# Kernel optimization log

Measured on AMD Instinct MI355X. Metric: run time of the kernel, lower is better.

The kernel has to match this reference:

```python
import jax, jax.numpy as jnp
import numpy as np

N = 20000           # graph nodes == vocab_size
E_RAND = 160000     # random edges (avg degree 8)
E = E_RAND + N      # + self loops (dgl.add_self_loop)
B, S, D = 16, 512, 768
IN_DIM, HID, HEADS = 4, 16, 8
GRID = 10010
NEG_SLOPE = 0.2


def _zero_row0(t):
    # padding_idx=0 in nn.Embedding -> row 0 is zeros
    return t.at[0].set(0.0)


def setup_inputs() -> dict:
    key = jax.random.key(0)
    ks = jax.random.split(key, 20)
    self_loops = jnp.arange(N, dtype=jnp.int64 if jax.config.x64_enabled else jnp.int32)
    edge_src = jax.random.randint(ks[0], (E,), 0, N).at[E_RAND:].set(self_loops)
    edge_dst = jax.random.randint(ks[1], (E,), 0, N).at[E_RAND:].set(self_loops)
    inp = {
        "trj_token": jax.random.randint(ks[2], (B, S), 0, N),
        "min_list": jax.random.randint(ks[3], (B, S), 0, 1441),
        "weekday_list": jax.random.randint(ks[4], (B, S), 0, 8),
        "day_list": jax.random.randint(ks[5], (B, S), 0, 367),
        "grid_list": jax.random.randint(ks[6], (B, S), 0, GRID),
        "poi_list": jax.random.randint(ks[7], (B, S), 0, 5),
        "edge_src": edge_src,
        "edge_dst": edge_dst,
        "feature": jax.random.normal(ks[8], (N, IN_DIM), jnp.float32),
        "W_src1": jax.random.normal(ks[9], (IN_DIM, HEADS, HID), jnp.float32) * 0.3,
        "W_dst1": jax.random.normal(ks[10], (IN_DIM, HEADS, HID), jnp.float32) * 0.3,
        "attn1": jax.random.normal(ks[11], (HEADS, HID), jnp.float32) * 0.3,
        "W_src2": jax.random.normal(ks[12], (HEADS * HID, 1, D), jnp.float32) * 0.05,
        "W_dst2": jax.random.normal(ks[13], (HEADS * HID, 1, D), jnp.float32) * 0.05,
        "attn2": jax.random.normal(ks[14], (1, D), jnp.float32) * 0.05,
        "grid_table": _zero_row0(jax.random.normal(ks[15], (GRID, D), jnp.float32)),
        "daytime_table": _zero_row0(jax.random.normal(ks[16], (1441, D), jnp.float32)),
        "weekday_table": _zero_row0(jax.random.normal(ks[17], (8, D), jnp.float32)),
        "day_table": _zero_row0(jax.random.normal(ks[18], (367, D), jnp.float32)),
    }
    return inp


def gatv2_layer(x, es, ed, W_s, W_d, attn):
    # GATv2: score_e = attn . leaky_relu(Wsrc x[src] + Wdst x[dst]); edge-softmax over dst
    hs = jnp.einsum('nd,dhf->nhf', x, W_s)           # [N,H,F]
    hd = jnp.einsum('nd,dhf->nhf', x, W_d)           # [N,H,F]
    e = jax.nn.leaky_relu(hs[es] + hd[ed], NEG_SLOPE)  # [E,H,F]
    score = jnp.einsum('ehf,hf->eh', e, attn)        # [E,H]
    m = jax.lax.stop_gradient(jax.ops.segment_max(score, ed, num_segments=N))
    ex = jnp.exp(score - m[ed])
    denom = jax.ops.segment_sum(ex, ed, num_segments=N)  # [N,H]
    alpha = ex / denom[ed]                           # [E,H]
    msg = alpha[..., None] * hs[es]                  # [E,H,F]
    return jax.ops.segment_sum(msg, ed, num_segments=N)  # [N,H,F]


def positional_embedding(seq_len, d_model):
    pos = jnp.arange(seq_len, dtype=jnp.float32)[:, None]
    div = jnp.exp(jnp.arange(0, d_model, 2, dtype=jnp.float32) * (-np.log(10000.0) / d_model))
    pe = jnp.zeros((seq_len, d_model), jnp.float32)
    pe = pe.at[:, 0::2].set(jnp.sin(pos * div))
    pe = pe.at[:, 1::2].set(jnp.cos(pos * div))
    return pe[None]  # [1,S,D]


def reference(trj_token, min_list, weekday_list, day_list, grid_list, poi_list,
              edge_src, edge_dst, feature,
              W_src1, W_dst1, attn1, W_src2, W_dst2, attn2,
              grid_table, daytime_table, weekday_table, day_table):
    # GAT2: two GATv2 layers over the road-network graph
    h1 = gatv2_layer(feature, edge_src, edge_dst, W_src1, W_dst1, attn1)   # [N,8,16]
    h1 = jax.nn.elu(h1.reshape(N, HEADS * HID))                            # concat heads
    h2 = gatv2_layer(h1, edge_src, edge_dst, W_src2, W_dst2, attn2)        # [N,1,768]
    node_emb = h2[:, 0, :]                                                 # [N,768]

    token = node_emb[trj_token]                                            # [B,S,D]
    time_emb = (weekday_table[weekday_list]
                + daytime_table[min_list]
                + day_table[day_list])
    grid_emb = grid_table[grid_list]
    pe = positional_embedding(trj_token.shape[1], D)
    return pe + token + time_emb + grid_emb
```

## Files before the change

### kernel.cpp

```cpp
#include <hip/hip_runtime.h>
#include <hip/hip_bf16.h>

#define N_NODES 20000
#define N_EDGES 180000
#define D_OUT   768
#define D_H1    128
#define B_SZ    16
#define S_LEN   512
#define NEG_SLOPE_C 0.2f

typedef __attribute__((ext_vector_type(8))) short bf16x8;
typedef __attribute__((ext_vector_type(4))) float f32x4;

__device__ __forceinline__ float leaky1(float x){ return x >= 0.0f ? x : NEG_SLOPE_C * x; }
__device__ __forceinline__ unsigned short f2bf(float x){
  union { __hip_bfloat16 h; unsigned short u; } v; v.h = __float2bfloat16(x); return v.u;
}
__device__ __forceinline__ float bf2f(unsigned short u){
  return __uint_as_float(((unsigned)u) << 16);
}
__device__ __forceinline__ float4 bf4_to_f4(ushort4 u){
  return make_float4(bf2f(u.x), bf2f(u.y), bf2f(u.z), bf2f(u.w));
}
__device__ __forceinline__ ushort4 f4_to_bf4(float4 v){
  ushort4 u; u.x=f2bf(v.x); u.y=f2bf(v.y); u.z=f2bf(v.z); u.w=f2bf(v.w); return u;
}

__device__ __forceinline__ float score12(const float4&u0,const float4&u1,const float4&u2,
                                         const float4&h0,const float4&h1,const float4&h2v,
                                         const float4&a0,const float4&a1,const float4&a2){
  return leaky1(u0.x+h0.x)*a0.x + leaky1(u0.y+h0.y)*a0.y
       + leaky1(u0.z+h0.z)*a0.z + leaky1(u0.w+h0.w)*a0.w
       + leaky1(u1.x+h1.x)*a1.x + leaky1(u1.y+h1.y)*a1.y
       + leaky1(u1.z+h1.z)*a1.z + leaky1(u1.w+h1.w)*a1.w
       + leaky1(u2.x+h2v.x)*a2.x + leaky1(u2.y+h2v.y)*a2.y
       + leaky1(u2.z+h2v.z)*a2.z + leaky1(u2.w+h2v.w)*a2.w;
}
__device__ __forceinline__ void rescale_if(float mn, float&m, float&den,
                                           float4&a0,float4&a1,float4&a2){
  if(mn > m){
    float r = expf(m - mn);
    den *= r;
    a0.x*=r; a0.y*=r; a0.z*=r; a0.w*=r;
    a1.x*=r; a1.y*=r; a1.z*=r; a1.w*=r;
    a2.x*=r; a2.y*=r; a2.z*=r; a2.w*=r;
    m = mn;
  }
}
__device__ __forceinline__ void axpy12(float w, const float4&u0,const float4&u1,const float4&u2,
                                       float4&a0,float4&a1,float4&a2){
  a0.x+=w*u0.x; a0.y+=w*u0.y; a0.z+=w*u0.z; a0.w+=w*u0.w;
  a1.x+=w*u1.x; a1.y+=w*u1.y; a1.z+=w*u1.z; a1.w+=w*u1.w;
  a2.x+=w*u2.x; a2.y+=w*u2.y; a2.z+=w*u2.z; a2.w+=w*u2.w;
}
__device__ __forceinline__ void edge_pair(const unsigned short* __restrict__ hs2,
    const int* __restrict__ es, const int* __restrict__ eidx, int k, int l,
    const float4&h0,const float4&h1,const float4&h2v,
    const float4&w0,const float4&w1,const float4&w2,
    float&m,float&den,float4&a0,float4&a1,float4&a2){
  int e0=eidx[k], e1=eidx[k+1];
  const ushort4* p0=(const ushort4*)(hs2+(size_t)es[e0]*D_OUT);
  const ushort4* p1=(const ushort4*)(hs2+(size_t)es[e1]*D_OUT);
  float4 u0=bf4_to_f4(p0[l]),u1=bf4_to_f4(p0[64+l]),u2=bf4_to_f4(p0[128+l]);
  float4 v0=bf4_to_f4(p1[l]),v1=bf4_to_f4(p1[64+l]),v2=bf4_to_f4(p1[128+l]);
  float s0=score12(u0,u1,u2,h0,h1,h2v,w0,w1,w2);
  float s1=score12(v0,v1,v2,h0,h1,h2v,w0,w1,w2);
  #pragma unroll
  for(int off=1; off<64; off<<=1){ s0+=__shfl_xor(s0,off,64); s1+=__shfl_xor(s1,off,64); }
  float mn=fmaxf(m,fmaxf(s0,s1));
  rescale_if(mn,m,den,a0,a1,a2);
  float q0=expf(s0-m), q1=expf(s1-m);
  den+=q0+q1;
  axpy12(q0,u0,u1,u2,a0,a1,a2);
  axpy12(q1,v0,v1,v2,a0,a1,a2);
}
__device__ __forceinline__ void edge_one(const unsigned short* __restrict__ hs2,
    const int* __restrict__ es, const int* __restrict__ eidx, int k, int l,
    const float4&h0,const float4&h1,const float4&h2v,
    const float4&w0,const float4&w1,const float4&w2,
    float&m,float&den,float4&a0,float4&a1,float4&a2){
  int e0=eidx[k];
  const ushort4* p0=(const ushort4*)(hs2+(size_t)es[e0]*D_OUT);
  float4 u0=bf4_to_f4(p0[l]),u1=bf4_to_f4(p0[64+l]),u2=bf4_to_f4(p0[128+l]);
  float s0=score12(u0,u1,u2,h0,h1,h2v,w0,w1,w2);
  #pragma unroll
  for(int off=1; off<64; off<<=1) s0+=__shfl_xor(s0,off,64);
  float mn=fmaxf(m,s0);
  rescale_if(mn,m,den,a0,a1,a2);
  float q0=expf(s0-m);
  den+=q0;
  axpy12(q0,u0,u1,u2,a0,a1,a2);
}

__global__ void k_count(const int* __restrict__ ed, int* __restrict__ deg){
  int e = blockIdx.x*256 + threadIdx.x;
  if(e < N_EDGES) atomicAdd(&deg[ed[e]], 1);
}

__global__ void k_scan(const int* __restrict__ deg, int* __restrict__ row_ptr, int* __restrict__ cursor){
  __shared__ int part[256];
  int t = threadIdx.x;
  const int CH = (N_NODES + 255) / 256;
  int base = t * CH;
  int s = 0;
  for(int i=0;i<CH;i++){ int n = base+i; if(n < N_NODES) s += deg[n]; }
  part[t] = s;
  __syncthreads();
  for(int off=1; off<256; off<<=1){
    int v = (t >= off) ? part[t-off] : 0;
    __syncthreads();
    part[t] += v;
    __syncthreads();
  }
  int run = (t==0) ? 0 : part[t-1];
  for(int i=0;i<CH;i++){
    int n = base+i;
    if(n < N_NODES){ row_ptr[n] = run; cursor[n] = run; run += deg[n]; }
  }
  if(t == 255) row_ptr[N_NODES] = run;
}

__global__ void k_scatter(const int* __restrict__ ed, int* __restrict__ cursor, int* __restrict__ eidx){
  int e = blockIdx.x*256 + threadIdx.x;
  if(e < N_EDGES){
    int pos = atomicAdd(&cursor[ed[e]], 1);
    eidx[pos] = e;
  }
}

__global__ void k_gemm1(const float* __restrict__ feat, const float* __restrict__ Ws,
                        const float* __restrict__ Wd,
                        unsigned short* __restrict__ hs1, unsigned short* __restrict__ hd1){
  int idx = blockIdx.x*256 + threadIdx.x;
  if(idx >= N_NODES*D_H1) return;
  int n = idx >> 7, hf = idx & 127;
  float f0 = feat[n*4+0], f1 = feat[n*4+1], f2 = feat[n*4+2], f3 = feat[n*4+3];
  hs1[idx] = f2bf(f0*Ws[hf] + f1*Ws[128+hf] + f2*Ws[256+hf] + f3*Ws[384+hf]);
  hd1[idx] = f2bf(f0*Wd[hf] + f1*Wd[128+hf] + f2*Wd[256+hf] + f3*Wd[384+hf]);
}

__global__ void k_fused1(const unsigned short* __restrict__ hs1, const unsigned short* __restrict__ hd1,
                         const int* __restrict__ es, const int* __restrict__ row_ptr,
                         const int* __restrict__ eidx, const float* __restrict__ attn1,
                         unsigned short* __restrict__ h1){
  int node = blockIdx.x*4 + (threadIdx.x >> 6);
  int l = threadIdx.x & 63;
  if(node >= N_NODES) return;
  int rp = row_ptr[node], re = row_ptr[node+1];
  float hda = bf2f(hd1[(size_t)node*D_H1 + l]);
  float hdb = bf2f(hd1[(size_t)node*D_H1 + 64 + l]);
  float awa = attn1[l], awb = attn1[64 + l];
  float m0 = -INFINITY, m1 = -INFINITY;
  float d0 = 0.f, d1 = 0.f, a0 = 0.f, a1 = 0.f;
  int k = rp;
  for(; k+1 < re; k += 2){
    int e0 = eidx[k], e1 = eidx[k+1];
    int s0 = es[e0],  s1 = es[e1];
    float xa0 = bf2f(hs1[(size_t)s0*D_H1 + l]);
    float xb0 = bf2f(hs1[(size_t)s0*D_H1 + 64 + l]);
    float xa1 = bf2f(hs1[(size_t)s1*D_H1 + l]);
    float xb1 = bf2f(hs1[(size_t)s1*D_H1 + 64 + l]);
    float ta0 = leaky1(xa0 + hda) * awa;
    float tb0 = leaky1(xb0 + hdb) * awb;
    float ta1 = leaky1(xa1 + hda) * awa;
    float tb1 = leaky1(xb1 + hdb) * awb;
    #pragma unroll
    for(int off=1; off<16; off<<=1){
      ta0 += __shfl_xor(ta0, off, 64);
      tb0 += __shfl_xor(tb0, off, 64);
      ta1 += __shfl_xor(ta1, off, 64);
      tb1 += __shfl_xor(tb1, off, 64);
    }
    float mn0 = fmaxf(m0, fmaxf(ta0, ta1));
    float mn1 = fmaxf(m1, fmaxf(tb0, tb1));
    float r0 = expf(m0 - mn0), r1 = expf(m1 - mn1);
    float wa0 = expf(ta0 - mn0), wa1 = expf(ta1 - mn0);
    float wb0 = expf(tb0 - mn1), wb1 = expf(tb1 - mn1);
    d0 = d0*r0 + wa0 + wa1;
    d1 = d1*r1 + wb0 + wb1;
    a0 = a0*r0 + wa0*xa0 + wa1*xa1;
    a1 = a1*r1 + wb0*xb0 + wb1*xb1;
    m0 = mn0; m1 = mn1;
  }
  if(k < re){
    int e = eidx[k]; int s = es[e];
    float xa = bf2f(hs1[(size_t)s*D_H1 + l]);
    float xb = bf2f(hs1[(size_t)s*D_H1 + 64 + l]);
    float t0 = leaky1(xa + hda) * awa;
    float t1 = leaky1(xb + hdb) * awb;
    #pragma unroll
    for(int off=1; off<16; off<<=1){
      t0 += __shfl_xor(t0, off, 64);
      t1 += __shfl_xor(t1, off, 64);
    }
    float mn0 = fmaxf(m0, t0), mn1 = fmaxf(m1, t1);
    float r0 = expf(m0 - mn0), r1 = expf(m1 - mn1);
    float w0 = expf(t0 - mn0), w1 = expf(t1 - mn1);
    d0 = d0*r0 + w0;      d1 = d1*r1 + w1;
    a0 = a0*r0 + w0*xa;   a1 = a1*r1 + w1*xb;
    m0 = mn0; m1 = mn1;
  }
  float v0 = a0 / d0, v1 = a1 / d1;
  v0 = v0 > 0.f ? v0 : expm1f(v0);
  v1 = v1 > 0.f ? v1 : expm1f(v1);
  h1[(size_t)node*D_H1 + l]      = f2bf(v0);
  h1[(size_t)node*D_H1 + 64 + l] = f2bf(v1);
}

__global__ void k_wprep(const float* __restrict__ Ws, const float* __restrict__ Wd,
                        unsigned short* __restrict__ WtS, unsigned short* __restrict__ WtD){
  int i = blockIdx.x*256 + threadIdx.x;
  if(i >= D_OUT*D_H1) return;
  int c = i >> 7, k = i & 127;
  WtS[i] = f2bf(Ws[(size_t)k*D_OUT + c]);
  WtD[i] = f2bf(Wd[(size_t)k*D_OUT + c]);
}

__global__ __launch_bounds__(256) void k_gemm2m(const unsigned short* __restrict__ h1b,
                        const unsigned short* __restrict__ WtS, const unsigned short* __restrict__ WtD,
                        unsigned short* __restrict__ hs2, unsigned short* __restrict__ hd2){
  int wave = threadIdx.x >> 6, lane = threadIdx.x & 63;
  int wr = wave >> 1, wc = wave & 1;
  int m0 = blockIdx.x*64 + wr*32;
  int c0 = blockIdx.y*128 + wc*64;
  int lr = lane & 15, lk = lane >> 4;

  f32x4 acc[2][4][2];
  #pragma unroll
  for(int a=0;a<2;a++)
    #pragma unroll
    for(int j=0;j<4;j++)
      #pragma unroll
      for(int mmat=0;mmat<2;mmat++)
        acc[a][j][mmat] = (f32x4){0.f,0.f,0.f,0.f};

  int ra0 = m0 + lr;      if(ra0 > N_NODES-1) ra0 = N_NODES-1;
  int ra1 = m0 + 16 + lr; if(ra1 > N_NODES-1) ra1 = N_NODES-1;
  const unsigned short* pa0 = h1b + (size_t)ra0*D_H1 + lk*8;
  const unsigned short* pa1 = h1b + (size_t)ra1*D_H1 + lk*8;

  #pragma unroll
  for(int t=0;t<4;t++){
    bf16x8 a0 = *(const bf16x8*)(pa0 + t*32);
    bf16x8 a1 = *(const bf16x8*)(pa1 + t*32);
    #pragma unroll
    for(int j=0;j<4;j++){
      size_t bo = (size_t)(c0 + j*16 + lr)*D_H1 + t*32 + lk*8;
      bf16x8 bs = *(const bf16x8*)(WtS + bo);
      bf16x8 bd = *(const bf16x8*)(WtD + bo);
      acc[0][j][0] = __builtin_amdgcn_mfma_f32_16x16x32_bf16(a0, bs, acc[0][j][0], 0, 0, 0);
      acc[1][j][0] = __builtin_amdgcn_mfma_f32_16x16x32_bf16(a1, bs, acc[1][j][0], 0, 0, 0);
      acc[0][j][1] = __builtin_amdgcn_mfma_f32_16x16x32_bf16(a0, bd, acc[0][j][1], 0, 0, 0);
      acc[1][j][1] = __builtin_amdgcn_mfma_f32_16x16x32_bf16(a1, bd, acc[1][j][1], 0, 0, 0);
    }
  }

  #pragma unroll
  for(int a=0;a<2;a++){
    #pragma unroll
    for(int r=0;r<4;r++){
      int row = m0 + a*16 + lk*4 + r;
      if(row < N_NODES){
        size_t base = (size_t)row*D_OUT;
        #pragma unroll
        for(int j=0;j<4;j++){
          int col = c0 + j*16 + lr;
          hs2[base + col] = f2bf(acc[a][j][0][r]);
          hd2[base + col] = f2bf(acc[a][j][1][r]);
        }
      }
    }
  }
}

__global__ __launch_bounds__(256) void k_fused2(const unsigned short* __restrict__ hs2,
                         const unsigned short* __restrict__ hd2,
                         const int* __restrict__ es, const int* __restrict__ row_ptr,
                         const int* __restrict__ eidx, const float* __restrict__ attn2,
                         unsigned short* __restrict__ h2){
  int wv = threadIdx.x >> 6, l = threadIdx.x & 63;
  int nA = blockIdx.x*8 + wv*2;
  int nB = nA + 1;
  if(nA >= N_NODES) return;
  bool hasB = (nB < N_NODES);

  const float4* pa = (const float4*)attn2;
  float4 aw0 = pa[l], aw1 = pa[64+l], aw2 = pa[128+l];
  const ushort4* pdA = (const ushort4*)(hd2 + (size_t)nA*D_OUT);
  float4 hA0 = bf4_to_f4(pdA[l]), hA1 = bf4_to_f4(pdA[64+l]), hA2 = bf4_to_f4(pdA[128+l]);
  float4 hB0, hB1, hB2;
  if(hasB){
    const ushort4* pdB = (const ushort4*)(hd2 + (size_t)nB*D_OUT);
    hB0 = bf4_to_f4(pdB[l]); hB1 = bf4_to_f4(pdB[64+l]); hB2 = bf4_to_f4(pdB[128+l]);
  } else { hB0 = hB1 = hB2 = make_float4(0,0,0,0); }

  int kA = row_ptr[nA], reA = row_ptr[nA+1];
  int kB = hasB ? row_ptr[nB] : 0, reB = hasB ? row_ptr[nB+1] : 0;

  float mA = -INFINITY, dA = 0.f;
  float mB = -INFINITY, dB = 0.f;
  float4 aA0 = make_float4(0,0,0,0), aA1 = aA0, aA2 = aA0;
  float4 aB0 = aA0, aB1 = aA0, aB2 = aA0;

  while(kA+1 < reA && kB+1 < reB){
    int eA0 = eidx[kA], eA1 = eidx[kA+1], eB0 = eidx[kB], eB1 = eidx[kB+1];
    const ushort4* p0 = (const ushort4*)(hs2 + (size_t)es[eA0]*D_OUT);
    const ushort4* p1 = (const ushort4*)(hs2 + (size_t)es[eA1]*D_OUT);
    const ushort4* p2 = (const ushort4*)(hs2 + (size_t)es[eB0]*D_OUT);
    const ushort4* p3 = (const ushort4*)(hs2 + (size_t)es[eB1]*D_OUT);
    float4 uA0=bf4_to_f4(p0[l]), uA1=bf4_to_f4(p0[64+l]), uA2=bf4_to_f4(p0[128+l]);
    float4 vA0=bf4_to_f4(p1[l]), vA1=bf4_to_f4(p1[64+l]), vA2=bf4_to_f4(p1[128+l]);
    float4 uB0=bf4_to_f4(p2[l]), uB1=bf4_to_f4(p2[64+l]), uB2=bf4_to_f4(p2[128+l]);
    float4 vB0=bf4_to_f4(p3[l]), vB1=bf4_to_f4(p3[64+l]), vB2=bf4_to_f4(p3[128+l]);
    float s0 = score12(uA0,uA1,uA2, hA0,hA1,hA2, aw0,aw1,aw2);
    float s1 = score12(vA0,vA1,vA2, hA0,hA1,hA2, aw0,aw1,aw2);
    float s2 = score12(uB0,uB1,uB2, hB0,hB1,hB2, aw0,aw1,aw2);
    float s3 = score12(vB0,vB1,vB2, hB0,hB1,hB2, aw0,aw1,aw2);
    #pragma unroll
    for(int off=1; off<64; off<<=1){
      s0 += __shfl_xor(s0, off, 64);
      s1 += __shfl_xor(s1, off, 64);
      s2 += __shfl_xor(s2, off, 64);
      s3 += __shfl_xor(s3, off, 64);
    }
    float mnA = fmaxf(mA, fmaxf(s0, s1));
    rescale_if(mnA, mA, dA, aA0, aA1, aA2);
    float qa0 = expf(s0 - mA), qa1 = expf(s1 - mA);
    dA += qa0 + qa1;
    axpy12(qa0, uA0,uA1,uA2, aA0,aA1,aA2);
    axpy12(qa1, vA0,vA1,vA2, aA0,aA1,aA2);
    float mnB = fmaxf(mB, fmaxf(s2, s3));
    rescale_if(mnB, mB, dB, aB0, aB1, aB2);
    float qb0 = expf(s2 - mB), qb1 = expf(s3 - mB);
    dB += qb0 + qb1;
    axpy12(qb0, uB0,uB1,uB2, aB0,aB1,aB2);
    axpy12(qb1, vB0,vB1,vB2, aB0,aB1,aB2);
    kA += 2; kB += 2;
  }
  while(kA+1 < reA){ edge_pair(hs2, es, eidx, kA, l, hA0,hA1,hA2, aw0,aw1,aw2, mA,dA,aA0,aA1,aA2); kA += 2; }
  while(kB+1 < reB){ edge_pair(hs2, es, eidx, kB, l, hB0,hB1,hB2, aw0,aw1,aw2, mB,dB,aB0,aB1,aB2); kB += 2; }
  if(kA < reA) edge_one(hs2, es, eidx, kA, l, hA0,hA1,hA2, aw0,aw1,aw2, mA,dA,aA0,aA1,aA2);
  if(kB < reB) edge_one(hs2, es, eidx, kB, l, hB0,hB1,hB2, aw0,aw1,aw2, mB,dB,aB0,aB1,aB2);

  {
    float rd = 1.f/dA;
    ushort4* po = (ushort4*)(h2 + (size_t)nA*D_OUT);
    aA0.x*=rd; aA0.y*=rd; aA0.z*=rd; aA0.w*=rd;
    aA1.x*=rd; aA1.y*=rd; aA1.z*=rd; aA1.w*=rd;
    aA2.x*=rd; aA2.y*=rd; aA2.z*=rd; aA2.w*=rd;
    po[l] = f4_to_bf4(aA0); po[64+l] = f4_to_bf4(aA1); po[128+l] = f4_to_bf4(aA2);
  }
  if(hasB){
    float rd = 1.f/dB;
    ushort4* po = (ushort4*)(h2 + (size_t)nB*D_OUT);
    aB0.x*=rd; aB0.y*=rd; aB0.z*=rd; aB0.w*=rd;
    aB1.x*=rd; aB1.y*=rd; aB1.z*=rd; aB1.w*=rd;
    aB2.x*=rd; aB2.y*=rd; aB2.z*=rd; aB2.w*=rd;
    po[l] = f4_to_bf4(aB0); po[64+l] = f4_to_bf4(aB1); po[128+l] = f4_to_bf4(aB2);
  }
}

__global__ __launch_bounds__(192) void k_out(const unsigned short* __restrict__ h2,
    const int* __restrict__ tok, const int* __restrict__ mins, const int* __restrict__ wkd,
    const int* __restrict__ dayl, const int* __restrict__ grd,
    const float* __restrict__ grid_t, const float* __restrict__ dayt_t,
    const float* __restrict__ week_t, const float* __restrict__ day_t,
    float* __restrict__ out){
  int bs = blockIdx.x;
  int t  = threadIdx.x;
  int s  = bs & (S_LEN-1);
  int tk = tok[bs], mn = mins[bs], wk = wkd[bs], dy = dayl[bs], gr = grd[bs];
  float4 r = bf4_to_f4(((const ushort4*)(h2 + (size_t)tk*D_OUT))[t]);
  float4 v;
  v = ((const float4*)(week_t + (size_t)wk*D_OUT))[t]; r.x+=v.x; r.y+=v.y; r.z+=v.z; r.w+=v.w;
  v = ((const float4*)(dayt_t + (size_t)mn*D_OUT))[t]; r.x+=v.x; r.y+=v.y; r.z+=v.z; r.w+=v.w;
  v = ((const float4*)(day_t  + (size_t)dy*D_OUT))[t]; r.x+=v.x; r.y+=v.y; r.z+=v.z; r.w+=v.w;
  v = ((const float4*)(grid_t + (size_t)gr*D_OUT))[t]; r.x+=v.x; r.y+=v.y; r.z+=v.z; r.w+=v.w;
  const float K = 0.011992630692677313f;
  float d0 = expf(-K * (float)(4*t));
  float d1 = expf(-K * (float)(4*t+2));
  float sf = (float)s;
  r.x += sinf(sf*d0); r.y += cosf(sf*d0);
  r.z += sinf(sf*d1); r.w += cosf(sf*d1);
  ((float4*)(out + (size_t)bs*D_OUT))[t] = r;
}

extern "C" void kernel_launch(void* const* d_in, const int* in_sizes, int n_in,
                              void* d_out, int out_size, void* d_ws, size_t ws_size,
                              hipStream_t stream) {
  const int*   trj   = (const int*)  d_in[0];
  const int*   mins  = (const int*)  d_in[1];
  const int*   wkd   = (const int*)  d_in[2];
  const int*   dayl  = (const int*)  d_in[3];
  const int*   grd   = (const int*)  d_in[4];
  const int*   es    = (const int*)  d_in[6];
  const int*   ed    = (const int*)  d_in[7];
  const float* feat  = (const float*)d_in[8];
  const float* Ws1   = (const float*)d_in[9];
  const float* Wd1   = (const float*)d_in[10];
  const float* attn1 = (const float*)d_in[11];
  const float* Ws2   = (const float*)d_in[12];
  const float* Wd2   = (const float*)d_in[13];
  const float* attn2 = (const float*)d_in[14];
  const float* gridt = (const float*)d_in[15];
  const float* daytt = (const float*)d_in[16];
  const float* weekt = (const float*)d_in[17];
  const float* dayt  = (const float*)d_in[18];
  float* out = (float*)d_out;

  char* ws = (char*)d_ws;
  size_t off = 0;
  auto alloc = [&](size_t bytes)->char*{
    char* p = ws + off;
    off += bytes;
    off = (off + 255) & ~(size_t)255;
    return p;
  };
  unsigned short* hs1 = (unsigned short*)alloc((size_t)N_NODES*D_H1*2);
  unsigned short* hd1 = (unsigned short*)alloc((size_t)N_NODES*D_H1*2);
  unsigned short* h1  = (unsigned short*)alloc((size_t)N_NODES*D_H1*2);
  unsigned short* WtS = (unsigned short*)alloc((size_t)D_OUT*D_H1*2);
  unsigned short* WtD = (unsigned short*)alloc((size_t)D_OUT*D_H1*2);
  unsigned short* hs2 = (unsigned short*)alloc((size_t)N_NODES*D_OUT*2);
  unsigned short* hd2 = (unsigned short*)alloc((size_t)N_NODES*D_OUT*2);
  unsigned short* h2  = (unsigned short*)alloc((size_t)N_NODES*D_OUT*2);
  int* deg      = (int*)alloc((size_t)N_NODES*4);
  int* row_ptr  = (int*)alloc((size_t)(N_NODES+1)*4);
  int* cursor   = (int*)alloc((size_t)N_NODES*4);
  int* eidx     = (int*)alloc((size_t)N_EDGES*4);

  hipMemsetAsync(deg, 0, (size_t)N_NODES*4, stream);
  k_count  <<<(N_EDGES+255)/256, 256, 0, stream>>>(ed, deg);
  k_scan   <<<1, 256, 0, stream>>>(deg, row_ptr, cursor);
  k_scatter<<<(N_EDGES+255)/256, 256, 0, stream>>>(ed, cursor, eidx);

  k_gemm1 <<<(N_NODES*D_H1)/256, 256, 0, stream>>>(feat, Ws1, Wd1, hs1, hd1);
  k_fused1<<<(N_NODES+3)/4, 256, 0, stream>>>(hs1, hd1, es, row_ptr, eidx, attn1, h1);

  k_wprep <<<(D_OUT*D_H1+255)/256, 256, 0, stream>>>(Ws2, Wd2, WtS, WtD);
  dim3 g2((N_NODES+63)/64, D_OUT/128);
  k_gemm2m<<<g2, 256, 0, stream>>>(h1, WtS, WtD, hs2, hd2);
  k_fused2<<<(N_NODES+7)/8, 256, 0, stream>>>(hs2, hd2, es, row_ptr, eidx, attn2, h2);

  k_out<<<B_SZ*S_LEN, 192, 0, stream>>>(h2, trj, mins, wkd, dayl, grd,
                                        gridt, daytt, weekt, dayt, out);
}
```

Baseline: 363.6 us.

## Store source ids in CSR, preload neighbor lists per wave, one node per wave

The scatter step now writes the source node id directly into the CSR array, which removes the eidx→es double indirection in both aggregation kernels. Each wave loads up to 64 neighbor ids with one coalesced read and hands them out with shuffles, falling back to global loads when the degree exceeds 64. k_fused2 goes from two interleaved nodes per wave to one node per wave with twice as many blocks. This trades the memory-level parallelism of interleaving two nodes for simpler code and more waves.

```diff
diff --git a/kernel.cpp b/kernel.cpp
--- a/kernel.cpp
+++ b/kernel.cpp
@@ -53,14 +53,13 @@
   a1.x+=w*u1.x; a1.y+=w*u1.y; a1.z+=w*u1.z; a1.w+=w*u1.w;
   a2.x+=w*u2.x; a2.y+=w*u2.y; a2.z+=w*u2.z; a2.w+=w*u2.w;
 }
-__device__ __forceinline__ void edge_pair(const unsigned short* __restrict__ hs2,
-    const int* __restrict__ es, const int* __restrict__ eidx, int k, int l,
+__device__ __forceinline__ void f2_pair(const unsigned short* __restrict__ hs2,
+    int s0i, int s1i, int l,
     const float4&h0,const float4&h1,const float4&h2v,
     const float4&w0,const float4&w1,const float4&w2,
     float&m,float&den,float4&a0,float4&a1,float4&a2){
-  int e0=eidx[k], e1=eidx[k+1];
-  const ushort4* p0=(const ushort4*)(hs2+(size_t)es[e0]*D_OUT);
-  const ushort4* p1=(const ushort4*)(hs2+(size_t)es[e1]*D_OUT);
+  const ushort4* p0=(const ushort4*)(hs2+(size_t)s0i*D_OUT);
+  const ushort4* p1=(const ushort4*)(hs2+(size_t)s1i*D_OUT);
   float4 u0=bf4_to_f4(p0[l]),u1=bf4_to_f4(p0[64+l]),u2=bf4_to_f4(p0[128+l]);
   float4 v0=bf4_to_f4(p1[l]),v1=bf4_to_f4(p1[64+l]),v2=bf4_to_f4(p1[128+l]);
   float s0=score12(u0,u1,u2,h0,h1,h2v,w0,w1,w2);
@@ -74,13 +73,12 @@
   axpy12(q0,u0,u1,u2,a0,a1,a2);
   axpy12(q1,v0,v1,v2,a0,a1,a2);
 }
-__device__ __forceinline__ void edge_one(const unsigned short* __restrict__ hs2,
-    const int* __restrict__ es, const int* __restrict__ eidx, int k, int l,
+__device__ __forceinline__ void f2_one(const unsigned short* __restrict__ hs2,
+    int s0i, int l,
     const float4&h0,const float4&h1,const float4&h2v,
     const float4&w0,const float4&w1,const float4&w2,
     float&m,float&den,float4&a0,float4&a1,float4&a2){
-  int e0=eidx[k];
-  const ushort4* p0=(const ushort4*)(hs2+(size_t)es[e0]*D_OUT);
+  const ushort4* p0=(const ushort4*)(hs2+(size_t)s0i*D_OUT);
   float4 u0=bf4_to_f4(p0[l]),u1=bf4_to_f4(p0[64+l]),u2=bf4_to_f4(p0[128+l]);
   float s0=score12(u0,u1,u2,h0,h1,h2v,w0,w1,w2);
   #pragma unroll
@@ -120,11 +118,12 @@
   if(t == 255) row_ptr[N_NODES] = run;
 }
 
-__global__ void k_scatter(const int* __restrict__ ed, int* __restrict__ cursor, int* __restrict__ eidx){
+__global__ void k_scatter(const int* __restrict__ es, const int* __restrict__ ed,
+                          int* __restrict__ cursor, int* __restrict__ sidx){
   int e = blockIdx.x*256 + threadIdx.x;
   if(e < N_EDGES){
     int pos = atomicAdd(&cursor[ed[e]], 1);
-    eidx[pos] = e;
+    sidx[pos] = es[e];
   }
 }
 
@@ -140,22 +139,27 @@
 }
 
 __global__ void k_fused1(const unsigned short* __restrict__ hs1, const unsigned short* __restrict__ hd1,
-                         const int* __restrict__ es, const int* __restrict__ row_ptr,
-                         const int* __restrict__ eidx, const float* __restrict__ attn1,
+                         const int* __restrict__ row_ptr, const int* __restrict__ sidx,
+                         const float* __restrict__ attn1,
                          unsigned short* __restrict__ h1){
   int node = blockIdx.x*4 + (threadIdx.x >> 6);
   int l = threadIdx.x & 63;
   if(node >= N_NODES) return;
   int rp = row_ptr[node], re = row_ptr[node+1];
+  int deg = re - rp;
   float hda = bf2f(hd1[(size_t)node*D_H1 + l]);
   float hdb = bf2f(hd1[(size_t)node*D_H1 + 64 + l]);
   float awa = attn1[l], awb = attn1[64 + l];
   float m0 = -INFINITY, m1 = -INFINITY;
   float d0 = 0.f, d1 = 0.f, a0 = 0.f, a1 = 0.f;
-  int k = rp;
-  for(; k+1 < re; k += 2){
-    int e0 = eidx[k], e1 = eidx[k+1];
-    int s0 = es[e0],  s1 = es[e1];
+
+  int sv = sidx[rp + ((l < deg) ? l : (deg-1))];
+  bool fast = (deg <= 64);
+
+  int k = 0;
+  for(; k+1 < deg; k += 2){
+    int s0 = fast ? __shfl(sv, k, 64)   : sidx[rp+k];
+    int s1 = fast ? __shfl(sv, k+1, 64) : sidx[rp+k+1];
     float xa0 = bf2f(hs1[(size_t)s0*D_H1 + l]);
     float xb0 = bf2f(hs1[(size_t)s0*D_H1 + 64 + l]);
     float xa1 = bf2f(hs1[(size_t)s1*D_H1 + l]);
@@ -182,8 +186,8 @@
     a1 = a1*r1 + wb0*xb0 + wb1*xb1;
     m0 = mn0; m1 = mn1;
   }
-  if(k < re){
-    int e = eidx[k]; int s = es[e];
+  if(k < deg){
+    int s = fast ? __shfl(sv, k, 64) : sidx[rp+k];
     float xa = bf2f(hs1[(size_t)s*D_H1 + l]);
     float xb = bf2f(hs1[(size_t)s*D_H1 + 64 + l]);
     float t0 = leaky1(xa + hda) * awa;
@@ -275,89 +279,43 @@
 
 __global__ __launch_bounds__(256) void k_fused2(const unsigned short* __restrict__ hs2,
                          const unsigned short* __restrict__ hd2,
-                         const int* __restrict__ es, const int* __restrict__ row_ptr,
-                         const int* __restrict__ eidx, const float* __restrict__ attn2,
+                         const int* __restrict__ row_ptr, const int* __restrict__ sidx,
+                         const float* __restrict__ attn2,
                          unsigned short* __restrict__ h2){
-  int wv = threadIdx.x >> 6, l = threadIdx.x & 63;
-  int nA = blockIdx.x*8 + wv*2;
-  int nB = nA + 1;
-  if(nA >= N_NODES) return;
-  bool hasB = (nB < N_NODES);
+  int node = blockIdx.x*4 + (threadIdx.x >> 6);
+  int l = threadIdx.x & 63;
+  if(node >= N_NODES) return;
+  int rp = row_ptr[node], re = row_ptr[node+1];
+  int deg = re - rp;
 
   const float4* pa = (const float4*)attn2;
   float4 aw0 = pa[l], aw1 = pa[64+l], aw2 = pa[128+l];
-  const ushort4* pdA = (const ushort4*)(hd2 + (size_t)nA*D_OUT);
-  float4 hA0 = bf4_to_f4(pdA[l]), hA1 = bf4_to_f4(pdA[64+l]), hA2 = bf4_to_f4(pdA[128+l]);
-  float4 hB0, hB1, hB2;
-  if(hasB){
-    const ushort4* pdB = (const ushort4*)(hd2 + (size_t)nB*D_OUT);
-    hB0 = bf4_to_f4(pdB[l]); hB1 = bf4_to_f4(pdB[64+l]); hB2 = bf4_to_f4(pdB[128+l]);
-  } else { hB0 = hB1 = hB2 = make_float4(0,0,0,0); }
-
-  int kA = row_ptr[nA], reA = row_ptr[nA+1];
-  int kB = hasB ? row_ptr[nB] : 0, reB = hasB ? row_ptr[nB+1] : 0;
-
-  float mA = -INFINITY, dA = 0.f;
-  float mB = -INFINITY, dB = 0.f;
-  float4 aA0 = make_float4(0,0,0,0), aA1 = aA0, aA2 = aA0;
-  float4 aB0 = aA0, aB1 = aA0, aB2 = aA0;
-
-  while(kA+1 < reA && kB+1 < reB){
-    int eA0 = eidx[kA], eA1 = eidx[kA+1], eB0 = eidx[kB], eB1 = eidx[kB+1];
-    const ushort4* p0 = (const ushort4*)(hs2 + (size_t)es[eA0]*D_OUT);
-    const ushort4* p1 = (const ushort4*)(hs2 + (size_t)es[eA1]*D_OUT);
-    const ushort4* p2 = (const ushort4*)(hs2 + (size_t)es[eB0]*D_OUT);
-    const ushort4* p3 = (const ushort4*)(hs2 + (size_t)es[eB1]*D_OUT);
-    float4 uA0=bf4_to_f4(p0[l]), uA1=bf4_to_f4(p0[64+l]), uA2=bf4_to_f4(p0[128+l]);
-    float4 vA0=bf4_to_f4(p1[l]), vA1=bf4_to_f4(p1[64+l]), vA2=bf4_to_f4(p1[128+l]);
-    float4 uB0=bf4_to_f4(p2[l]), uB1=bf4_to_f4(p2[64+l]), uB2=bf4_to_f4(p2[128+l]);
-    float4 vB0=bf4_to_f4(p3[l]), vB1=bf4_to_f4(p3[64+l]), vB2=bf4_to_f4(p3[128+l]);
-    float s0 = score12(uA0,uA1,uA2, hA0,hA1,hA2, aw0,aw1,aw2);
-    float s1 = score12(vA0,vA1,vA2, hA0,hA1,hA2, aw0,aw1,aw2);
-    float s2 = score12(uB0,uB1,uB2, hB0,hB1,hB2, aw0,aw1,aw2);
-    float s3 = score12(vB0,vB1,vB2, hB0,hB1,hB2, aw0,aw1,aw2);
-    #pragma unroll
-    for(int off=1; off<64; off<<=1){
-      s0 += __shfl_xor(s0, off, 64);
-      s1 += __shfl_xor(s1, off, 64);
-      s2 += __shfl_xor(s2, off, 64);
-      s3 += __shfl_xor(s3, off, 64);
-    }
-    float mnA = fmaxf(mA, fmaxf(s0, s1));
-    rescale_if(mnA, mA, dA, aA0, aA1, aA2);
-    float qa0 = expf(s0 - mA), qa1 = expf(s1 - mA);
-    dA += qa0 + qa1;
-    axpy12(qa0, uA0,uA1,uA2, aA0,aA1,aA2);
-    axpy12(qa1, vA0,vA1,vA2, aA0,aA1,aA2);
-    float mnB = fmaxf(mB, fmaxf(s2, s3));
-    rescale_if(mnB, mB, dB, aB0, aB1, aB2);
-    float qb0 = expf(s2 - mB), qb1 = expf(s3 - mB);
-    dB += qb0 + qb1;
-    axpy12(qb0, uB0,uB1,uB2, aB0,aB1,aB2);
-    axpy12(qb1, vB0,vB1,vB2, aB0,aB1,aB2);
-    kA += 2; kB += 2;
-  }
-  while(kA+1 < reA){ edge_pair(hs2, es, eidx, kA, l, hA0,hA1,hA2, aw0,aw1,aw2, mA,dA,aA0,aA1,aA2); kA += 2; }
-  while(kB+1 < reB){ edge_pair(hs2, es, eidx, kB, l, hB0,hB1,hB2, aw0,aw1,aw2, mB,dB,aB0,aB1,aB2); kB += 2; }
-  if(kA < reA) edge_one(hs2, es, eidx, kA, l, hA0,hA1,hA2, aw0,aw1,aw2, mA,dA,aA0,aA1,aA2);
-  if(kB < reB) edge_one(hs2, es, eidx, kB, l, hB0,hB1,hB2, aw0,aw1,aw2, mB,dB,aB0,aB1,aB2);
-
-  {
-    float rd = 1.f/dA;
-    ushort4* po = (ushort4*)(h2 + (size_t)nA*D_OUT);
-    aA0.x*=rd; aA0.y*=rd; aA0.z*=rd; aA0.w*=rd;
-    aA1.x*=rd; aA1.y*=rd; aA1.z*=rd; aA1.w*=rd;
-    aA2.x*=rd; aA2.y*=rd; aA2.z*=rd; aA2.w*=rd;
-    po[l] = f4_to_bf4(aA0); po[64+l] = f4_to_bf4(aA1); po[128+l] = f4_to_bf4(aA2);
-  }
-  if(hasB){
-    float rd = 1.f/dB;
-    ushort4* po = (ushort4*)(h2 + (size_t)nB*D_OUT);
-    aB0.x*=rd; aB0.y*=rd; aB0.z*=rd; aB0.w*=rd;
-    aB1.x*=rd; aB1.y*=rd; aB1.z*=rd; aB1.w*=rd;
-    aB2.x*=rd; aB2.y*=rd; aB2.z*=rd; aB2.w*=rd;
-    po[l] = f4_to_bf4(aB0); po[64+l] = f4_to_bf4(aB1); po[128+l] = f4_to_bf4(aB2);
-  }
+  const ushort4* pd = (const ushort4*)(hd2 + (size_t)node*D_OUT);
+  float4 hd0 = bf4_to_f4(pd[l]), hd1v = bf4_to_f4(pd[64+l]), hd2v = bf4_to_f4(pd[128+l]);
+
+  int sv = sidx[rp + ((l < deg) ? l : (deg-1))];
+  bool fast = (deg <= 64);
+
+  float m = -INFINITY, den = 0.f;
+  float4 ac0 = make_float4(0,0,0,0), ac1 = ac0, ac2 = ac0;
+
+  int k = 0;
+  for(; k+1 < deg; k += 2){
+    int s0 = fast ? __shfl(sv, k, 64)   : sidx[rp+k];
+    int s1 = fast ? __shfl(sv, k+1, 64) : sidx[rp+k+1];
+    f2_pair(hs2, s0, s1, l, hd0, hd1v, hd2v, aw0, aw1, aw2, m, den, ac0, ac1, ac2);
+  }
+  if(k < deg){
+    int s0 = fast ? __shfl(sv, k, 64) : sidx[rp+k];
+    f2_one(hs2, s0, l, hd0, hd1v, hd2v, aw0, aw1, aw2, m, den, ac0, ac1, ac2);
+  }
+
+  float rd = 1.f/den;
+  ushort4* po = (ushort4*)(h2 + (size_t)node*D_OUT);
+  ac0.x*=rd; ac0.y*=rd; ac0.z*=rd; ac0.w*=rd;
+  ac1.x*=rd; ac1.y*=rd; ac1.z*=rd; ac1.w*=rd;
+  ac2.x*=rd; ac2.y*=rd; ac2.z*=rd; ac2.w*=rd;
+  po[l] = f4_to_bf4(ac0); po[64+l] = f4_to_bf4(ac1); po[128+l] = f4_to_bf4(ac2);
 }
 
 __global__ __launch_bounds__(192) void k_out(const unsigned short* __restrict__ h2,
@@ -427,20 +385,20 @@
   int* deg      = (int*)alloc((size_t)N_NODES*4);
   int* row_ptr  = (int*)alloc((size_t)(N_NODES+1)*4);
   int* cursor   = (int*)alloc((size_t)N_NODES*4);
-  int* eidx     = (int*)alloc((size_t)N_EDGES*4);
+  int* sidx     = (int*)alloc((size_t)N_EDGES*4);
 
   hipMemsetAsync(deg, 0, (size_t)N_NODES*4, stream);
   k_count  <<<(N_EDGES+255)/256, 256, 0, stream>>>(ed, deg);
   k_scan   <<<1, 256, 0, stream>>>(deg, row_ptr, cursor);
-  k_scatter<<<(N_EDGES+255)/256, 256, 0, stream>>>(ed, cursor, eidx);
+  k_scatter<<<(N_EDGES+255)/256, 256, 0, stream>>>(es, ed, cursor, sidx);
 
   k_gemm1 <<<(N_NODES*D_H1)/256, 256, 0, stream>>>(feat, Ws1, Wd1, hs1, hd1);
-  k_fused1<<<(N_NODES+3)/4, 256, 0, stream>>>(hs1, hd1, es, row_ptr, eidx, attn1, h1);
+  k_fused1<<<(N_NODES+3)/4, 256, 0, stream>>>(hs1, hd1, row_ptr, sidx, attn1, h1);
 
   k_wprep <<<(D_OUT*D_H1+255)/256, 256, 0, stream>>>(Ws2, Wd2, WtS, WtD);
   dim3 g2((N_NODES+63)/64, D_OUT/128);
   k_gemm2m<<<g2, 256, 0, stream>>>(h1, WtS, WtD, hs2, hd2);
-  k_fused2<<<(N_NODES+7)/8, 256, 0, stream>>>(hs2, hd2, es, row_ptr, eidx, attn2, h2);
+  k_fused2<<<(N_NODES+3)/4, 256, 0, stream>>>(hs2, hd2, row_ptr, sidx, attn2, h2);
 
   k_out<<<B_SZ*S_LEN, 192, 0, stream>>>(h2, trj, mins, wkd, dayl, grd,
                                         gridt, daytt, weekt, dayt, out);
```

Result: faster. 339.2 us (-6.7%).
